# Kernel optimization log

Hardware: AMD Instinct MI355X
Metric: run time of the kernel (lower is better)

## Reference

```python
import jax, jax.numpy as jnp
import numpy as np

N_NODES = 50000
N_EDGES = 3200000
N_GRAPHS = 50
IN_FEATS, HIDDEN, OUT_FEATS = 5, 64, 2


def setup_inputs() -> dict:
    key = jax.random.key(0)
    ks = jax.random.split(key, 10)
    x = jax.random.normal(ks[0], (N_NODES, IN_FEATS), dtype=jnp.float32)
    edge_index = jax.random.randint(ks[1], (2, N_EDGES), 0, N_NODES, dtype=jnp.int64)
    edge_attr = jax.random.uniform(ks[2], (N_EDGES, 1), dtype=jnp.float32)
    batch = jnp.sort(jax.random.randint(ks[3], (N_NODES,), 0, N_GRAPHS, dtype=jnp.int64))
    s1 = 1.0 / np.sqrt(IN_FEATS)
    s2 = 1.0 / np.sqrt(HIDDEN)
    W1 = jax.random.uniform(ks[4], (IN_FEATS, HIDDEN), jnp.float32, -s1, s1)
    b1 = jnp.zeros((HIDDEN,), jnp.float32)
    W2 = jax.random.uniform(ks[5], (HIDDEN, HIDDEN), jnp.float32, -s2, s2)
    b2 = jnp.zeros((HIDDEN,), jnp.float32)
    Wo = jax.random.uniform(ks[6], (HIDDEN, OUT_FEATS), jnp.float32, -s2, s2)
    bo = jax.random.uniform(ks[7], (OUT_FEATS,), jnp.float32, -s2, s2)
    return {"x": x, "edge_index": edge_index, "edge_attr": edge_attr, "batch": batch,
            "W1": W1, "b1": b1, "W2": W2, "b2": b2, "Wo": Wo, "bo": bo}


def _gcn_conv(x, src, dst, ew, W, b):
    # symmetric normalization: D^{-1/2} (A + I) D^{-1/2}, weighted degrees
    deg = jax.ops.segment_sum(ew, dst, num_segments=N_NODES)
    dinv = jnp.where(deg > 0, jax.lax.rsqrt(jnp.where(deg > 0, deg, 1.0)), 0.0)
    norm = dinv[src] * ew * dinv[dst]  # [E+N]
    h = x @ W                           # transform before propagate (PyG order)
    msg = h[src] * norm[:, None]        # gather + scale per edge
    out = jax.ops.segment_sum(msg, dst, num_segments=N_NODES)
    return out + b


def reference(x, edge_index, edge_attr, batch, W1, b1, W2, b2, Wo, bo):
    ew = edge_attr.squeeze(-1)
    loop = jnp.arange(N_NODES, dtype=edge_index.dtype)  # add self-loops (GCNConv default)
    src = jnp.concatenate([edge_index[0], loop])
    dst = jnp.concatenate([edge_index[1], loop])
    ew = jnp.concatenate([ew, jnp.ones((N_NODES,), ew.dtype)])
    h = jax.nn.relu(_gcn_conv(x, src, dst, ew, W1, b1))
    h = jax.nn.relu(_gcn_conv(h, src, dst, ew, W2, b2))
    # global mean pool over graphs
    sums = jax.ops.segment_sum(h, batch, num_segments=N_GRAPHS)
    cnt = jax.ops.segment_sum(jnp.ones((N_NODES,), h.dtype), batch, num_segments=N_GRAPHS)
    pooled = sums / jnp.maximum(cnt, 1.0)[:, None]
    return pooled @ Wo + bo  # [N_GRAPHS, OUT_FEATS]
```

## Files before the change

kernel.cpp:

```cpp
#include <hip/hip_runtime.h>
#include <hip/hip_fp16.h>

#define N_NODES 50000
#define N_EDGES 3200000
#define N_GRAPHS 50
#define IN_F 5
#define HID 64
#define OUT_F 2

#define BK2_SHIFT 7
#define BK2_W 128
#define NBKT2 391
#define NB1 250
#define EPB 12800
#define TILE 6400
#define SLOTS 7
#define CAP2 9216
#define NBIN2 128
#define NWAVE 8192

__global__ __launch_bounds__(1024) void k_bhist(const int* dst, int* total) {
    __shared__ int hist[NBKT2];
    int t = threadIdx.x, blk = blockIdx.x;
    for (int b = t; b < NBKT2; b += 1024) hist[b] = 0;
    __syncthreads();
    int base = blk * EPB;
    for (int k = t; k < EPB; k += 1024)
        atomicAdd(&hist[__builtin_nontemporal_load(&dst[base + k]) >> BK2_SHIFT], 1);
    __syncthreads();
    for (int b = t; b < NBKT2; b += 1024) {
        int h = hist[b];
        if (h) atomicAdd(&total[b], h);
    }
}

__global__ void k_bscanB(const int* total, int* rpB, int* cursor) {
    __shared__ int s[256];
    int t = threadIdx.x;
    int v[2], sum = 0;
#pragma unroll
    for (int j = 0; j < 2; ++j) {
        int idx = t * 2 + j;
        v[j] = (idx < NBKT2) ? total[idx] : 0;
        sum += v[j];
    }
    s[t] = sum;
    __syncthreads();
    for (int off = 1; off < 256; off <<= 1) {
        int a = (t >= off) ? s[t - off] : 0;
        __syncthreads();
        s[t] += a;
        __syncthreads();
    }
    int run = s[t] - sum;
#pragma unroll
    for (int j = 0; j < 2; ++j) {
        int idx = t * 2 + j;
        if (idx < NBKT2) { rpB[idx] = run; cursor[idx] = run; }
        run += v[j];
    }
    if (t == 0) rpB[NBKT2] = N_EDGES;
}

__global__ __launch_bounds__(1024) void k_bucket(const int* src, const int* dst,
                        const float* ew, int* cursor, int* key4, unsigned short* wh2) {
    __shared__ int keyb[TILE];
    __shared__ unsigned short whb[TILE];
    __shared__ int hist[NBKT2];
    __shared__ int soff[NBKT2];
    __shared__ int delta[NBKT2];
    __shared__ int s[512];
    int t = threadIdx.x, blk = blockIdx.x;
    for (int tile = 0; tile < EPB / TILE; ++tile) {
        int base = blk * EPB + tile * TILE;
        for (int b = t; b < NBKT2; b += 1024) hist[b] = 0;
        __syncthreads();
        int ky[SLOTS]; unsigned short wv[SLOTS]; int rk[SLOTS];
#pragma unroll
        for (int i = 0; i < SLOTS; ++i) {
            int k = t + i * 1024;
            if (k < TILE) {
                int d  = __builtin_nontemporal_load(&dst[base + k]);
                int sv = __builtin_nontemporal_load(&src[base + k]);
                float w = __builtin_nontemporal_load(&ew[base + k]);
                ky[i] = sv | (d << 16);
                wv[i] = __half_as_ushort(__float2half(w));
                rk[i] = atomicAdd(&hist[d >> BK2_SHIFT], 1);
            }
        }
        __syncthreads();
        if (t < 512) s[t] = (t < NBKT2) ? hist[t] : 0;
        __syncthreads();
        for (int off = 1; off < 512; off <<= 1) {
            int a = (t < 512 && t >= off) ? s[t - off] : 0;
            __syncthreads();
            if (t < 512) s[t] += a;
            __syncthreads();
        }
        if (t < NBKT2) {
            int h = hist[t];
            soff[t] = s[t] - h;
            if (h) delta[t] = atomicAdd(&cursor[t], h) - soff[t];
        }
        __syncthreads();
#pragma unroll
        for (int i = 0; i < SLOTS; ++i) {
            int k = t + i * 1024;
            if (k < TILE) {
                int b = ((unsigned)ky[i] >> 16) >> BK2_SHIFT;
                int p = soff[b] + rk[i];
                keyb[p] = ky[i];
                whb[p] = wv[i];
            }
        }
        __syncthreads();
#pragma unroll
        for (int i = 0; i < SLOTS; ++i) {
            int k = t + i * 1024;
            if (k < TILE) {
                int u = keyb[k];
                int b = ((unsigned)u >> 16) >> BK2_SHIFT;
                int gp = k + delta[b];
                key4[gp] = u;
                wh2[gp] = whb[k];
            }
        }
        __syncthreads();
    }
}

__global__ __launch_bounds__(1024) void k_bsort2(const int* rpB, int* key4,
                      const unsigned short* wh2, const float* x,
                      int* rp2, int* rp2e, float* dinv, __half* xp) {
    __shared__ int keybuf[CAP2];
    __shared__ unsigned short whbuf[CAP2];
    __shared__ int hist[NBIN2];
    __shared__ int binoff[NBIN2];
    __shared__ int s[NBIN2];
    __shared__ float wd[NBIN2];
    int t = threadIdx.x, b = blockIdx.x;
    int e0 = rpB[b], cnt = rpB[b + 1] - e0;
    if (t < NBIN2) { hist[t] = 0; wd[t] = 0.f; }
    __syncthreads();
    for (int k = t; k < cnt; k += 1024) {
        int u = key4[e0 + k];
        unsigned short wh = wh2[e0 + k];
        keybuf[k] = u; whbuf[k] = wh;
        int dl = ((unsigned)u >> 16) & (BK2_W - 1);
        atomicAdd(&hist[dl], 1);
        atomicAdd(&wd[dl], __half2float(__ushort_as_half(wh)));
    }
    __syncthreads();
    if (t < NBIN2) s[t] = hist[t];
    __syncthreads();
    for (int off = 1; off < NBIN2; off <<= 1) {
        int a = (t < NBIN2 && t >= off) ? s[t - off] : 0;
        __syncthreads();
        if (t < NBIN2) s[t] += a;
        __syncthreads();
    }
    if (t < NBIN2) {
        binoff[t] = s[t] - hist[t];
        int node = (b << BK2_SHIFT) + t;
        if (node < N_NODES) {
            rp2[node]  = e0 + s[t] - hist[t];
            rp2e[node] = e0 + s[t];
            float di = rsqrtf(1.0f + wd[t]);
            dinv[node] = di;
            const float* xi = &x[node * IN_F];
            __half* o = &xp[node * 8];
#pragma unroll
            for (int f = 0; f < IN_F; ++f) o[f] = __float2half(xi[f] * di);
            o[5] = o[6] = o[7] = __float2half(0.f);
        }
    }
    __syncthreads();
    for (int k = t; k < cnt; k += 1024) {
        int u = keybuf[k];
        int dl = ((unsigned)u >> 16) & (BK2_W - 1);
        int pos = atomicAdd(&binoff[dl], 1);
        key4[e0 + pos] = (u & 0xFFFF) | ((int)whbuf[k] << 16);
    }
}

__global__ void k_p(const int* rp2, const int* rp2e, const int* pk,
                    const __half* xp, const float* dinv, float* p) {
    int node = blockIdx.x * 4 + (threadIdx.x >> 6);
    int lane = threadIdx.x & 63;
    if (node >= N_NODES) return;
    int b = rp2[node], en = rp2e[node];
    float a0 = 0.f, a1 = 0.f, a2 = 0.f, a3 = 0.f, a4 = 0.f;
    for (int k = b + lane; k < en; k += 64) {
        int e = pk[k];
        float w = __half2float(__ushort_as_half((unsigned short)((unsigned)e >> 16)));
        const __half* xs = &xp[(e & 0xFFFF) * 8];
        int4 xv = *reinterpret_cast<const int4*>(xs);
        __half2 p01 = *(__half2*)&xv.x;
        __half2 p23 = *(__half2*)&xv.y;
        __half2 p45 = *(__half2*)&xv.z;
        a0 += w * __half2float(p01.x); a1 += w * __half2float(p01.y);
        a2 += w * __half2float(p23.x); a3 += w * __half2float(p23.y);
        a4 += w * __half2float(p45.x);
    }
    for (int off = 32; off; off >>= 1) {
        a0 += __shfl_down(a0, off); a1 += __shfl_down(a1, off); a2 += __shfl_down(a2, off);
        a3 += __shfl_down(a3, off); a4 += __shfl_down(a4, off);
    }
    if (lane == 0) {
        float di = dinv[node];
        const __half* xn = &xp[node * 8];
        float* pp = &p[node * IN_F];
        pp[0] = di * (a0 + __half2float(xn[0]));
        pp[1] = di * (a1 + __half2float(xn[1]));
        pp[2] = di * (a2 + __half2float(xn[2]));
        pp[3] = di * (a3 + __half2float(xn[3]));
        pp[4] = di * (a4 + __half2float(xn[4]));
    }
}

__global__ void k_h1g(const float* p, const float* W1, const float* b1,
                      const float* W2, const float* dinv,
                      unsigned char* g8u, float* rs) {
    __shared__ float W1s[IN_F * HID];
    __shared__ float W2s[HID * HID];
    __shared__ float b1s[HID];
    int t = threadIdx.x;
    for (int k = t; k < IN_F * HID; k += 256) W1s[k] = W1[k];
    for (int k = t; k < HID * HID; k += 256) W2s[k] = W2[k];
    if (t < HID) b1s[t] = b1[t];
    __syncthreads();
    int lane = t & 63;
    int wid = blockIdx.x * 4 + (t >> 6);
    int nw = gridDim.x * 4;
    for (int node = wid; node < N_NODES; node += nw) {
        const float* pp = &p[node * IN_F];
        float pv0 = pp[0], pv1 = pp[1], pv2 = pp[2], pv3 = pp[3], pv4 = pp[4];
        float h = b1s[lane] + pv0 * W1s[lane] + pv1 * W1s[64 + lane] + pv2 * W1s[128 + lane]
                + pv3 * W1s[192 + lane] + pv4 * W1s[256 + lane];
        h = fmaxf(h, 0.f);
        float acc = 0.f;
#pragma unroll
        for (int f = 0; f < HID; ++f) {
            float hf = __int_as_float(__builtin_amdgcn_readlane(__float_as_int(h), f));
            acc += hf * W2s[f * HID + lane];
        }
        float gv = acc * dinv[node];
        float am = fabsf(gv);
        for (int off = 32; off; off >>= 1) am = fmaxf(am, __shfl_xor(am, off));
        float inv = (am > 0.f) ? 127.0f / am : 0.f;
        g8u[node * HID + lane] = (unsigned char)(__float2int_rn(gv * inv) + 128);
        if (lane == 0) rs[node] = (am > 0.f) ? am * (1.0f / 127.0f) : 0.f;
    }
}

#define EDGE4_BODY(UU)                                                         \
    {                                                                          \
        int u_ = (UU);                                                         \
        float w_ = __half2float(__ushort_as_half((unsigned short)((unsigned)u_ >> 16))); \
        float wwv_ = w_ * rs[u_ & 0xFFFF];                                     \
        unsigned dw_ = *(const unsigned*)&g8u[(u_ & 0xFFFF) * HID + fo];       \
        a0 += wwv_ * (float)(dw_ & 0xFF);                                      \
        a1 += wwv_ * (float)((dw_ >> 8) & 0xFF);                               \
        a2 += wwv_ * (float)((dw_ >> 16) & 0xFF);                              \
        a3 += wwv_ * (float)(dw_ >> 24);                                       \
        sww += wwv_;                                                           \
    }

__global__ __launch_bounds__(256, 8) void k_h2g(const int* rp2, const int* rp2e,
                      const int* pk, const float* dinv, const unsigned char* g8u,
                      const float* rs, const float* b2, const int* batch, float* pool) {
    int t = threadIdx.x, lane = t & 63;
    int grp = lane >> 4;
    int fo = (lane & 15) << 2;
    int wid = blockIdx.x * 4 + (t >> 6);
    int n0 = (int)(((long long)wid * N_NODES) / NWAVE);
    int n1 = (int)(((long long)(wid + 1) * N_NODES) / NWAVE);
    if (n0 >= n1) return;
    float4 bj = *reinterpret_cast<const float4*>(&b2[fo]);
    float p0 = 0.f, p1 = 0.f, p2 = 0.f, p3 = 0.f;
    int cur = batch[n0];
    for (int node = n0; node < n1; ++node) {
        unsigned dws = *(const unsigned*)&g8u[node * HID + fo];
        float wq4 = 0.25f * rs[node];
        float a0 = wq4 * (float)(dws & 0xFF);
        float a1 = wq4 * (float)((dws >> 8) & 0xFF);
        float a2 = wq4 * (float)((dws >> 16) & 0xFF);
        float a3 = wq4 * (float)(dws >> 24);
        float sww = wq4;
        for (int k0 = rp2[node], e1 = rp2e[node]; k0 < e1; k0 += 64) {
            int kk = k0 + lane;
            int ev = (kk < e1) ? pk[kk] : 0;
            int m = e1 - k0; if (m > 64) m = 64;
            if (m == 64) {
#pragma unroll
                for (int q = 0; q < 16; ++q) EDGE4_BODY(__shfl(ev, (q << 2) | grp))
            } else {
                int ng = (m + 3) >> 2;
                for (int q = 0; q < ng; ++q) EDGE4_BODY(__shfl(ev, (q << 2) | grp))
            }
        }
#pragma unroll
        for (int off = 16; off <= 32; off <<= 1) {
            a0 += __shfl_xor(a0, off); a1 += __shfl_xor(a1, off);
            a2 += __shfl_xor(a2, off); a3 += __shfl_xor(a3, off);
            sww += __shfl_xor(sww, off);
        }
        float di = dinv[node];
        float corr = 128.0f * sww;
        float h0 = fmaxf(di * (a0 - corr) + bj.x, 0.f);
        float h1 = fmaxf(di * (a1 - corr) + bj.y, 0.f);
        float h2 = fmaxf(di * (a2 - corr) + bj.z, 0.f);
        float h3 = fmaxf(di * (a3 - corr) + bj.w, 0.f);
        int bb = batch[node];
        if (bb != cur) {
            if (lane < 16) {
                float* pb = &pool[cur * HID + fo];
                atomicAdd(pb + 0, p0); atomicAdd(pb + 1, p1);
                atomicAdd(pb + 2, p2); atomicAdd(pb + 3, p3);
            }
            cur = bb;
            p0 = p1 = p2 = p3 = 0.f;
        }
        p0 += h0; p1 += h1; p2 += h2; p3 += h3;
    }
    if (lane < 16) {
        float* pb = &pool[cur * HID + fo];
        atomicAdd(pb + 0, p0); atomicAdd(pb + 1, p1);
        atomicAdd(pb + 2, p2); atomicAdd(pb + 3, p3);
    }
}

__device__ int lowb(const int* a, int n, int v) {
    int lo = 0, hi = n;
    while (lo < hi) { int m = (lo + hi) >> 1; if (a[m] < v) lo = m + 1; else hi = m; }
    return lo;
}

__global__ void k_out(const float* pool, const int* batch, const float* Wo,
                      const float* bo, float* out) {
    int t = blockIdx.x * blockDim.x + threadIdx.x;
    if (t < N_GRAPHS * OUT_F) {
        int gi = t / OUT_F, k = t % OUT_F;
        int c = lowb(batch, N_NODES, gi + 1) - lowb(batch, N_NODES, gi);
        float cf = fmaxf((float)c, 1.0f);
        float acc = bo[k];
        for (int f = 0; f < HID; ++f)
            acc += (pool[gi * HID + f] / cf) * Wo[f * OUT_F + k];
        out[t] = acc;
    }
}

extern "C" void kernel_launch(void* const* d_in, const int* in_sizes, int n_in,
                              void* d_out, int out_size, void* d_ws, size_t ws_size,
                              hipStream_t stream) {
    const float* x   = (const float*)d_in[0];
    const int*   ei  = (const int*)d_in[1];
    const float* ea  = (const float*)d_in[2];
    const int*   bat = (const int*)d_in[3];
    const float* W1  = (const float*)d_in[4];
    const float* b1  = (const float*)d_in[5];
    const float* W2  = (const float*)d_in[6];
    const float* b2  = (const float*)d_in[7];
    const float* Wo  = (const float*)d_in[8];
    const float* bo  = (const float*)d_in[9];
    float* out = (float*)d_out;

    const int* src = ei;
    const int* dst = ei + N_EDGES;

    float* ws = (float*)d_ws;
    int*   rpB    = (int*)ws;
    int*   cursor = (int*)(ws + 400);
    int*   rp2    = (int*)(ws + 800);
    int*   rp2e   = (int*)(ws + 50816);
    float* dinv   = ws + 100832;
    float* rs     = ws + 150848;
    float* pool   = ws + 200864;
    int*   total  = (int*)(ws + 204064);
    float* p      = ws + 204464;
    int*   key4   = (int*)(ws + 454464);
    unsigned short* wh2 = (unsigned short*)(ws + 3654464);
    unsigned char* g8u = (unsigned char*)(ws + 5254464);
    __half* xp    = (__half*)(ws + 6054464);

    hipMemsetAsync(total, 0, NBKT2 * sizeof(int), stream);
    hipMemsetAsync(pool, 0, N_GRAPHS * HID * sizeof(float), stream);

    k_bhist <<<NB1, 1024, 0, stream>>>(dst, total);
    k_bscanB<<<1, 256, 0, stream>>>(total, rpB, cursor);
    k_bucket<<<NB1, 1024, 0, stream>>>(src, dst, ea, cursor, key4, wh2);
    k_bsort2<<<NBKT2, 1024, 0, stream>>>(rpB, key4, wh2, x, rp2, rp2e, dinv, xp);
    k_p     <<<(N_NODES + 3) / 4, 256, 0, stream>>>(rp2, rp2e, key4, xp, dinv, p);
    k_h1g   <<<1024, 256, 0, stream>>>(p, W1, b1, W2, dinv, g8u, rs);
    k_h2g   <<<NWAVE / 4, 256, 0, stream>>>(rp2, rp2e, key4, dinv, g8u, rs, b2, bat, pool);
    k_out   <<<1, 128, 0, stream>>>(pool, bat, Wo, bo, out);
}
```

Baseline: 288.2 us.

## Fuse layer-1 aggregation into h1 kernel, split bucket tiles, prefetch edges in h2

```diff
diff --git a/kernel.cpp b/kernel.cpp
--- a/kernel.cpp
+++ b/kernel.cpp
@@ -11,8 +11,9 @@
 #define BK2_SHIFT 7
 #define BK2_W 128
 #define NBKT2 391
-#define NB1 250
-#define EPB 12800
+#define NB_BH 250
+#define EPB_BH 12800
+#define NB_BK 500
 #define TILE 6400
 #define SLOTS 7
 #define CAP2 9216
@@ -24,8 +25,8 @@
     int t = threadIdx.x, blk = blockIdx.x;
     for (int b = t; b < NBKT2; b += 1024) hist[b] = 0;
     __syncthreads();
-    int base = blk * EPB;
-    for (int k = t; k < EPB; k += 1024)
+    int base = blk * EPB_BH;
+    for (int k = t; k < EPB_BH; k += 1024)
         atomicAdd(&hist[__builtin_nontemporal_load(&dst[base + k]) >> BK2_SHIFT], 1);
     __syncthreads();
     for (int b = t; b < NBKT2; b += 1024) {
@@ -70,68 +71,65 @@
     __shared__ int soff[NBKT2];
     __shared__ int delta[NBKT2];
     __shared__ int s[512];
-    int t = threadIdx.x, blk = blockIdx.x;
-    for (int tile = 0; tile < EPB / TILE; ++tile) {
-        int base = blk * EPB + tile * TILE;
-        for (int b = t; b < NBKT2; b += 1024) hist[b] = 0;
-        __syncthreads();
-        int ky[SLOTS]; unsigned short wv[SLOTS]; int rk[SLOTS];
-#pragma unroll
-        for (int i = 0; i < SLOTS; ++i) {
-            int k = t + i * 1024;
-            if (k < TILE) {
-                int d  = __builtin_nontemporal_load(&dst[base + k]);
-                int sv = __builtin_nontemporal_load(&src[base + k]);
-                float w = __builtin_nontemporal_load(&ew[base + k]);
-                ky[i] = sv | (d << 16);
-                wv[i] = __half_as_ushort(__float2half(w));
-                rk[i] = atomicAdd(&hist[d >> BK2_SHIFT], 1);
-            }
-        }
-        __syncthreads();
-        if (t < 512) s[t] = (t < NBKT2) ? hist[t] : 0;
-        __syncthreads();
-        for (int off = 1; off < 512; off <<= 1) {
-            int a = (t < 512 && t >= off) ? s[t - off] : 0;
-            __syncthreads();
-            if (t < 512) s[t] += a;
-            __syncthreads();
-        }
-        if (t < NBKT2) {
-            int h = hist[t];
-            soff[t] = s[t] - h;
-            if (h) delta[t] = atomicAdd(&cursor[t], h) - soff[t];
-        }
-        __syncthreads();
-#pragma unroll
-        for (int i = 0; i < SLOTS; ++i) {
-            int k = t + i * 1024;
-            if (k < TILE) {
-                int b = ((unsigned)ky[i] >> 16) >> BK2_SHIFT;
-                int p = soff[b] + rk[i];
-                keyb[p] = ky[i];
-                whb[p] = wv[i];
-            }
-        }
-        __syncthreads();
-#pragma unroll
-        for (int i = 0; i < SLOTS; ++i) {
-            int k = t + i * 1024;
-            if (k < TILE) {
-                int u = keyb[k];
-                int b = ((unsigned)u >> 16) >> BK2_SHIFT;
-                int gp = k + delta[b];
-                key4[gp] = u;
-                wh2[gp] = whb[k];
-            }
-        }
-        __syncthreads();
+    int t = threadIdx.x;
+    int base = blockIdx.x * TILE;
+    for (int b = t; b < NBKT2; b += 1024) hist[b] = 0;
+    __syncthreads();
+    int ky[SLOTS]; unsigned short wv[SLOTS]; int rk[SLOTS];
+#pragma unroll
+    for (int i = 0; i < SLOTS; ++i) {
+        int k = t + i * 1024;
+        if (k < TILE) {
+            int d  = __builtin_nontemporal_load(&dst[base + k]);
+            int sv = __builtin_nontemporal_load(&src[base + k]);
+            float w = __builtin_nontemporal_load(&ew[base + k]);
+            ky[i] = sv | (d << 16);
+            wv[i] = __half_as_ushort(__float2half(w));
+            rk[i] = atomicAdd(&hist[d >> BK2_SHIFT], 1);
+        }
+    }
+    __syncthreads();
+    if (t < 512) s[t] = (t < NBKT2) ? hist[t] : 0;
+    __syncthreads();
+    for (int off = 1; off < 512; off <<= 1) {
+        int a = (t < 512 && t >= off) ? s[t - off] : 0;
+        __syncthreads();
+        if (t < 512) s[t] += a;
+        __syncthreads();
+    }
+    if (t < NBKT2) {
+        int h = hist[t];
+        soff[t] = s[t] - h;
+        if (h) delta[t] = atomicAdd(&cursor[t], h) - soff[t];
+    }
+    __syncthreads();
+#pragma unroll
+    for (int i = 0; i < SLOTS; ++i) {
+        int k = t + i * 1024;
+        if (k < TILE) {
+            int b = ((unsigned)ky[i] >> 16) >> BK2_SHIFT;
+            int p = soff[b] + rk[i];
+            keyb[p] = ky[i];
+            whb[p] = wv[i];
+        }
+    }
+    __syncthreads();
+#pragma unroll
+    for (int i = 0; i < SLOTS; ++i) {
+        int k = t + i * 1024;
+        if (k < TILE) {
+            int u = keyb[k];
+            int b = ((unsigned)u >> 16) >> BK2_SHIFT;
+            int gp = k + delta[b];
+            key4[gp] = u;
+            wh2[gp] = whb[k];
+        }
     }
 }
 
 __global__ __launch_bounds__(1024) void k_bsort2(const int* rpB, int* key4,
                       const unsigned short* wh2, const float* x,
-                      int* rp2, int* rp2e, float* dinv, __half* xp) {
+                      int* rp2, float* dinv, __half* xp) {
     __shared__ int keybuf[CAP2];
     __shared__ unsigned short whbuf[CAP2];
     __shared__ int hist[NBIN2];
@@ -163,8 +161,7 @@
         binoff[t] = s[t] - hist[t];
         int node = (b << BK2_SHIFT) + t;
         if (node < N_NODES) {
-            rp2[node]  = e0 + s[t] - hist[t];
-            rp2e[node] = e0 + s[t];
+            rp2[node] = e0 + s[t] - hist[t];
             float di = rsqrtf(1.0f + wd[t]);
             dinv[node] = di;
             const float* xi = &x[node * IN_F];
@@ -174,6 +171,7 @@
             o[5] = o[6] = o[7] = __float2half(0.f);
         }
     }
+    if (b == NBKT2 - 1 && t == 0) rp2[N_NODES] = N_EDGES;
     __syncthreads();
     for (int k = t; k < cnt; k += 1024) {
         int u = keybuf[k];
@@ -183,43 +181,9 @@
     }
 }
 
-__global__ void k_p(const int* rp2, const int* rp2e, const int* pk,
-                    const __half* xp, const float* dinv, float* p) {
-    int node = blockIdx.x * 4 + (threadIdx.x >> 6);
-    int lane = threadIdx.x & 63;
-    if (node >= N_NODES) return;
-    int b = rp2[node], en = rp2e[node];
-    float a0 = 0.f, a1 = 0.f, a2 = 0.f, a3 = 0.f, a4 = 0.f;
-    for (int k = b + lane; k < en; k += 64) {
-        int e = pk[k];
-        float w = __half2float(__ushort_as_half((unsigned short)((unsigned)e >> 16)));
-        const __half* xs = &xp[(e & 0xFFFF) * 8];
-        int4 xv = *reinterpret_cast<const int4*>(xs);
-        __half2 p01 = *(__half2*)&xv.x;
-        __half2 p23 = *(__half2*)&xv.y;
-        __half2 p45 = *(__half2*)&xv.z;
-        a0 += w * __half2float(p01.x); a1 += w * __half2float(p01.y);
-        a2 += w * __half2float(p23.x); a3 += w * __half2float(p23.y);
-        a4 += w * __half2float(p45.x);
-    }
-    for (int off = 32; off; off >>= 1) {
-        a0 += __shfl_down(a0, off); a1 += __shfl_down(a1, off); a2 += __shfl_down(a2, off);
-        a3 += __shfl_down(a3, off); a4 += __shfl_down(a4, off);
-    }
-    if (lane == 0) {
-        float di = dinv[node];
-        const __half* xn = &xp[node * 8];
-        float* pp = &p[node * IN_F];
-        pp[0] = di * (a0 + __half2float(xn[0]));
-        pp[1] = di * (a1 + __half2float(xn[1]));
-        pp[2] = di * (a2 + __half2float(xn[2]));
-        pp[3] = di * (a3 + __half2float(xn[3]));
-        pp[4] = di * (a4 + __half2float(xn[4]));
-    }
-}
-
-__global__ void k_h1g(const float* p, const float* W1, const float* b1,
-                      const float* W2, const float* dinv,
+__global__ __launch_bounds__(256) void k_ph1g(const int* rp2, const int* pk,
+                      const __half* xp, const float* dinv, const float* W1,
+                      const float* b1, const float* W2,
                       unsigned char* g8u, float* rs) {
     __shared__ float W1s[IN_F * HID];
     __shared__ float W2s[HID * HID];
@@ -233,10 +197,34 @@
     int wid = blockIdx.x * 4 + (t >> 6);
     int nw = gridDim.x * 4;
     for (int node = wid; node < N_NODES; node += nw) {
-        const float* pp = &p[node * IN_F];
-        float pv0 = pp[0], pv1 = pp[1], pv2 = pp[2], pv3 = pp[3], pv4 = pp[4];
-        float h = b1s[lane] + pv0 * W1s[lane] + pv1 * W1s[64 + lane] + pv2 * W1s[128 + lane]
-                + pv3 * W1s[192 + lane] + pv4 * W1s[256 + lane];
+        int b = rp2[node], en = rp2[node + 1];
+        float a0 = 0.f, a1 = 0.f, a2 = 0.f, a3 = 0.f, a4 = 0.f;
+        for (int k = b + lane; k < en; k += 64) {
+            int e = pk[k];
+            float w = __half2float(__ushort_as_half((unsigned short)((unsigned)e >> 16)));
+            const __half* xs = &xp[(e & 0xFFFF) * 8];
+            int4 xv = *reinterpret_cast<const int4*>(xs);
+            __half2 p01 = *(__half2*)&xv.x;
+            __half2 p23 = *(__half2*)&xv.y;
+            __half2 p45 = *(__half2*)&xv.z;
+            a0 += w * __half2float(p01.x); a1 += w * __half2float(p01.y);
+            a2 += w * __half2float(p23.x); a3 += w * __half2float(p23.y);
+            a4 += w * __half2float(p45.x);
+        }
+        for (int off = 1; off < 64; off <<= 1) {
+            a0 += __shfl_xor(a0, off); a1 += __shfl_xor(a1, off);
+            a2 += __shfl_xor(a2, off); a3 += __shfl_xor(a3, off);
+            a4 += __shfl_xor(a4, off);
+        }
+        float di = dinv[node];
+        const __half* xn = &xp[node * 8];
+        float p0 = di * (a0 + __half2float(xn[0]));
+        float p1 = di * (a1 + __half2float(xn[1]));
+        float p2 = di * (a2 + __half2float(xn[2]));
+        float p3 = di * (a3 + __half2float(xn[3]));
+        float p4 = di * (a4 + __half2float(xn[4]));
+        float h = b1s[lane] + p0 * W1s[lane] + p1 * W1s[64 + lane] + p2 * W1s[128 + lane]
+                + p3 * W1s[192 + lane] + p4 * W1s[256 + lane];
         h = fmaxf(h, 0.f);
         float acc = 0.f;
 #pragma unroll
@@ -244,7 +232,7 @@
             float hf = __int_as_float(__builtin_amdgcn_readlane(__float_as_int(h), f));
             acc += hf * W2s[f * HID + lane];
         }
-        float gv = acc * dinv[node];
+        float gv = acc * di;
         float am = fabsf(gv);
         for (int off = 32; off; off >>= 1) am = fmaxf(am, __shfl_xor(am, off));
         float inv = (am > 0.f) ? 127.0f / am : 0.f;
@@ -253,7 +241,7 @@
     }
 }
 
-#define EDGE4_BODY(UU)                                                         \
+#define EDGE4_BODY_U(UU)                                                       \
     {                                                                          \
         int u_ = (UU);                                                         \
         float w_ = __half2float(__ushort_as_half((unsigned short)((unsigned)u_ >> 16))); \
@@ -266,7 +254,7 @@
         sww += wwv_;                                                           \
     }
 
-__global__ __launch_bounds__(256, 8) void k_h2g(const int* rp2, const int* rp2e,
+__global__ __launch_bounds__(256, 8) void k_h2g(const int* rp2,
                       const int* pk, const float* dinv, const unsigned char* g8u,
                       const float* rs, const float* b2, const int* batch, float* pool) {
     int t = threadIdx.x, lane = t & 63;
@@ -279,7 +267,12 @@
     float4 bj = *reinterpret_cast<const float4*>(&b2[fo]);
     float p0 = 0.f, p1 = 0.f, p2 = 0.f, p3 = 0.f;
     int cur = batch[n0];
+    int span_end = rp2[n1];
+    int kcur = rp2[n0];
+    int kk0 = kcur + lane;
+    int ev = (kk0 < N_EDGES) ? pk[kk0] : 0;
     for (int node = n0; node < n1; ++node) {
+        int e1 = rp2[node + 1];
         unsigned dws = *(const unsigned*)&g8u[node * HID + fo];
         float wq4 = 0.25f * rs[node];
         float a0 = wq4 * (float)(dws & 0xFF);
@@ -287,17 +280,30 @@
         float a2 = wq4 * (float)((dws >> 16) & 0xFF);
         float a3 = wq4 * (float)(dws >> 24);
         float sww = wq4;
-        for (int k0 = rp2[node], e1 = rp2e[node]; k0 < e1; k0 += 64) {
-            int kk = k0 + lane;
-            int ev = (kk < e1) ? pk[kk] : 0;
-            int m = e1 - k0; if (m > 64) m = 64;
+        while (kcur < e1) {
+            int m = e1 - kcur; if (m > 64) m = 64;
+            int knext = kcur + m;
+            int evn = 0;
+            if (knext < span_end) {
+                int kk2 = knext + lane;
+                evn = (kk2 < N_EDGES) ? pk[kk2] : 0;
+            }
             if (m == 64) {
 #pragma unroll
-                for (int q = 0; q < 16; ++q) EDGE4_BODY(__shfl(ev, (q << 2) | grp))
+                for (int q = 0; q < 16; ++q) {
+                    int u = __shfl(ev, (q << 2) | grp);
+                    EDGE4_BODY_U(u)
+                }
             } else {
                 int ng = (m + 3) >> 2;
-                for (int q = 0; q < ng; ++q) EDGE4_BODY(__shfl(ev, (q << 2) | grp))
+                for (int q = 0; q < ng; ++q) {
+                    int slot = (q << 2) | grp;
+                    int u = __shfl(ev, slot);
+                    if (slot >= m) u = 0;
+                    EDGE4_BODY_U(u)
+                }
             }
+            ev = evn; kcur = knext;
         }
 #pragma unroll
         for (int off = 16; off <= 32; off <<= 1) {
@@ -372,26 +378,23 @@
     int*   rpB    = (int*)ws;
     int*   cursor = (int*)(ws + 400);
     int*   rp2    = (int*)(ws + 800);
-    int*   rp2e   = (int*)(ws + 50816);
-    float* dinv   = ws + 100832;
-    float* rs     = ws + 150848;
-    float* pool   = ws + 200864;
-    int*   total  = (int*)(ws + 204064);
-    float* p      = ws + 204464;
-    int*   key4   = (int*)(ws + 454464);
-    unsigned short* wh2 = (unsigned short*)(ws + 3654464);
-    unsigned char* g8u = (unsigned char*)(ws + 5254464);
-    __half* xp    = (__half*)(ws + 6054464);
+    float* dinv   = ws + 50816;
+    float* rs     = ws + 100832;
+    float* pool   = ws + 150848;
+    int*   total  = (int*)(ws + 154048);
+    int*   key4   = (int*)(ws + 154448);
+    unsigned short* wh2 = (unsigned short*)(ws + 3354448);
+    unsigned char* g8u = (unsigned char*)(ws + 4954448);
+    __half* xp    = (__half*)(ws + 5754448);
 
     hipMemsetAsync(total, 0, NBKT2 * sizeof(int), stream);
     hipMemsetAsync(pool, 0, N_GRAPHS * HID * sizeof(float), stream);
 
-    k_bhist <<<NB1, 1024, 0, stream>>>(dst, total);
+    k_bhist <<<NB_BH, 1024, 0, stream>>>(dst, total);
     k_bscanB<<<1, 256, 0, stream>>>(total, rpB, cursor);
-    k_bucket<<<NB1, 1024, 0, stream>>>(src, dst, ea, cursor, key4, wh2);
-    k_bsort2<<<NBKT2, 1024, 0, stream>>>(rpB, key4, wh2, x, rp2, rp2e, dinv, xp);
-    k_p     <<<(N_NODES + 3) / 4, 256, 0, stream>>>(rp2, rp2e, key4, xp, dinv, p);
-    k_h1g   <<<1024, 256, 0, stream>>>(p, W1, b1, W2, dinv, g8u, rs);
-    k_h2g   <<<NWAVE / 4, 256, 0, stream>>>(rp2, rp2e, key4, dinv, g8u, rs, b2, bat, pool);
+    k_bucket<<<NB_BK, 1024, 0, stream>>>(src, dst, ea, cursor, key4, wh2);
+    k_bsort2<<<NBKT2, 1024, 0, stream>>>(rpB, key4, wh2, x, rp2, dinv, xp);
+    k_ph1g  <<<2048, 256, 0, stream>>>(rp2, key4, xp, dinv, W1, b1, W2, g8u, rs);
+    k_h2g   <<<NWAVE / 4, 256, 0, stream>>>(rp2, key4, dinv, g8u, rs, b2, bat, pool);
     k_out   <<<1, 128, 0, stream>>>(pool, bat, Wo, bo, out);
 }
```

Result: faster. 281.5 us (-2.3%).
